# Performance work log

Hardware: AMD Instinct MI355X
Metric: run time of the kernel (lower is better)

## Reference

```python
import jax, jax.numpy as jnp
import numpy as np

PREV_SIZE = 1024
SIZE = 4096
BATCH = 8192


def setup_inputs() -> dict:
    key = jax.random.key(0)
    k1, k2, k3, k4 = jax.random.split(key, 4)
    return {
        "prev_layer_output": jax.random.normal(k1, (PREV_SIZE, BATCH), dtype=jnp.float32),
        "input_A_weights": jax.random.normal(k2, (SIZE, PREV_SIZE), dtype=jnp.float32),
        "input_B_weights": jax.random.normal(k3, (SIZE, PREV_SIZE), dtype=jnp.float32),
        "table_weights": jax.random.normal(k4, (16, SIZE), dtype=jnp.float32),
    }


def reference(prev_layer_output, input_A_weights, input_B_weights, table_weights):
    # Soft input selection via row-softmax over previous neurons.
    pa = jax.nn.softmax(input_A_weights, axis=1)   # (size, prev_size)
    pb = jax.nn.softmax(input_B_weights, axis=1)   # (size, prev_size)
    pt = jax.nn.softmax(table_weights, axis=0)     # (16, size) softmax over gates

    A = pa @ prev_layer_output                     # (size, batch)
    B = pb @ prev_layer_output                     # (size, batch)
    AB = A * B

    p = pt[:, :, None]                             # (16, size, 1) broadcast over batch
    # Fused weighted sum over the 16 soft logic gates (no (16,size,batch) buffer).
    out = (
        p[1] * AB
        + p[2] * (A - AB)
        + p[3] * A
        + p[4] * (B - AB)
        + p[5] * B
        + p[6] * (A + B - 2.0 * AB)
        + p[7] * (A + B - AB)
        + p[8] * (1.0 - (A + B - AB))
        + p[9] * (1.0 - (A + B - 2.0 * AB))
        + p[10] * (1.0 - B)
        + p[11] * (1.0 - B + AB)
        + p[12] * (1.0 - A)
        + p[13] * (1.0 - A + AB)
        + p[14] * (1.0 - AB)
        + p[15]
    )
    return out
```

## Files before the change

kernel.cpp:

```cpp
#include <hip/hip_runtime.h>
#include <hip/hip_bf16.h>

#define K_DIM 1024
#define M_DIM 4096
#define N_DIM 8192
#define BK 64
#define BM 128
#define BN 256
#define NT 16

#define OFF_A 0
#define OFF_B (BM * BK)
#define OFF_P (2 * BM * BK)
#define BUF_ELEMS (2 * BM * BK + BN * BK)

typedef __attribute__((ext_vector_type(8))) __bf16 bf16x8_t;
typedef __attribute__((ext_vector_type(4))) float f32x4;

#define SBAR do { __builtin_amdgcn_sched_barrier(0); \
                  __builtin_amdgcn_s_barrier(); \
                  __builtin_amdgcn_sched_barrier(0); } while (0)
#define LGKM0 do { asm volatile("s_waitcnt lgkmcnt(0)" ::: "memory"); \
                   __builtin_amdgcn_sched_barrier(0); } while (0)
#define VMCNT(n) do { asm volatile("s_waitcnt vmcnt(" #n ")" ::: "memory"); \
                      __builtin_amdgcn_sched_barrier(0); } while (0)

__device__ inline unsigned short f2bf(float f) {
    unsigned u = __float_as_uint(f);
    u += 0x7FFF + ((u >> 16) & 1);
    return (unsigned short)(u >> 16);
}

__device__ __forceinline__ void gload_lds16(const void* g, void* l) {
    __builtin_amdgcn_global_load_lds(
        (const __attribute__((address_space(1))) unsigned int*)g,
        (__attribute__((address_space(3))) unsigned int*)l, 16, 0, 0);
}

__global__ void dual_softmax_kernel(const float* __restrict__ wa,
                                    const float* __restrict__ wb,
                                    unsigned short* __restrict__ pa,
                                    unsigned short* __restrict__ pb) {
    const int idx = blockIdx.x;
    const float* w = (idx < M_DIM) ? wa : wb;
    unsigned short* o = (idx < M_DIM) ? pa : pb;
    const int row = idx & (M_DIM - 1);
    const int tid = threadIdx.x;
    const float4 v = reinterpret_cast<const float4*>(w + (size_t)row * K_DIM)[tid];
    float m = fmaxf(fmaxf(v.x, v.y), fmaxf(v.z, v.w));
    #pragma unroll
    for (int off = 32; off >= 1; off >>= 1) m = fmaxf(m, __shfl_xor(m, off));
    __shared__ float redm[4];
    __shared__ float reds[4];
    if ((tid & 63) == 0) redm[tid >> 6] = m;
    __syncthreads();
    m = fmaxf(fmaxf(redm[0], redm[1]), fmaxf(redm[2], redm[3]));
    const float e0 = __expf(v.x - m), e1 = __expf(v.y - m);
    const float e2 = __expf(v.z - m), e3 = __expf(v.w - m);
    float s = e0 + e1 + e2 + e3;
    #pragma unroll
    for (int off = 32; off >= 1; off >>= 1) s += __shfl_xor(s, off);
    if ((tid & 63) == 0) reds[tid >> 6] = s;
    __syncthreads();
    s = reds[0] + reds[1] + reds[2] + reds[3];
    const float inv = 1.0f / s;
    ushort4 r;
    r.x = f2bf(e0 * inv); r.y = f2bf(e1 * inv);
    r.z = f2bf(e2 * inv); r.w = f2bf(e3 * inv);
    reinterpret_cast<ushort4*>(o + (size_t)row * K_DIM)[tid] = r;
}

__global__ void transpose_conv_kernel(const float* __restrict__ src,
                                      unsigned short* __restrict__ dst) {
    __shared__ float t[32][33];
    const int n0 = blockIdx.x * 32;
    const int k0 = blockIdx.y * 32;
    const int tx = threadIdx.x, ty = threadIdx.y;
    #pragma unroll
    for (int i = ty; i < 32; i += 8)
        t[i][tx] = src[(size_t)(k0 + i) * N_DIM + n0 + tx];
    __syncthreads();
    #pragma unroll
    for (int i = ty; i < 32; i += 8)
        dst[(size_t)(n0 + i) * K_DIM + k0 + tx] = f2bf(t[tx][i]);
}

__global__ void coef_kernel(const float* __restrict__ tw,
                            float4* __restrict__ coef) {
    const int r = blockIdx.x * 256 + threadIdx.x;
    float p[16];
    float m = -1e30f;
    #pragma unroll
    for (int k = 0; k < 16; ++k) { p[k] = tw[k * M_DIM + r]; m = fmaxf(m, p[k]); }
    float s = 0.f;
    #pragma unroll
    for (int k = 0; k < 16; ++k) { p[k] = __expf(p[k] - m); s += p[k]; }
    const float inv = 1.f / s;
    #pragma unroll
    for (int k = 0; k < 16; ++k) p[k] *= inv;
    const float cA  = p[2]+p[3]+p[6]+p[7]-p[8]-p[9]-p[12]-p[13];
    const float cB  = p[4]+p[5]+p[6]+p[7]-p[8]-p[9]-p[10]-p[11];
    const float cAB = p[1]-p[2]-p[4]-2.f*p[6]-p[7]+p[8]+2.f*p[9]+p[11]+p[13]-p[14];
    const float c0  = p[8]+p[9]+p[10]+p[11]+p[12]+p[13]+p[14]+p[15];
    coef[r] = make_float4(cA, cB, cAB, c0);
}

__device__ __forceinline__ void load_frags4(const unsigned short* lbase, int row0,
                                            int fk16, bf16x8_t (&f)[4]) {
    #pragma unroll
    for (int i = 0; i < 4; ++i) {
        const int row = row0 + i * 16;
        f[i] = *reinterpret_cast<const bf16x8_t*>(
            (const char*)lbase + row * 128 + ((fk16 ^ (row & 7)) * 16));
    }
}

__device__ __forceinline__ void mfma_block(const bf16x8_t (&a)[4], const bf16x8_t (&p)[4],
                                           f32x4 (&acc)[4][4]) {
    #pragma unroll
    for (int mi = 0; mi < 4; ++mi)
        #pragma unroll
        for (int ni = 0; ni < 4; ++ni)
            acc[mi][ni] = __builtin_amdgcn_mfma_f32_16x16x32_bf16(
                a[mi], p[ni], acc[mi][ni], 0, 0, 0);
}

__global__ __launch_bounds__(512, 2)
void dual_gemm_kernel(const unsigned short* __restrict__ pa,
                      const unsigned short* __restrict__ pb,
                      const unsigned short* __restrict__ pv,
                      const float4* __restrict__ coef,
                      float* __restrict__ out) {
    __shared__ unsigned short lds[2 * BUF_ELEMS];

    const int tid = threadIdx.x;
    const int lane = tid & 63;
    const int w = tid >> 6;
    const int wm = w >> 2, wn = w & 3;

    const int bm = blockIdx.y;
    const int bn = blockIdx.x;

    const int sub_row = lane >> 3;
    const int scol16  = (lane & 7) ^ sub_row;

    const unsigned short* gA = pa + (size_t)(bm * BM) * K_DIM;
    const unsigned short* gB = pb + (size_t)(bm * BM) * K_DIM;
    const unsigned short* gP = pv + (size_t)(bn * BN) * K_DIM;

    const int fr  = lane & 15;
    const int fkb = lane >> 4;
    const int arow0 = wm * 64 + fr;
    const int prow0 = wn * 64 + fr;

    f32x4 accA[4][4], accB[4][4];
    const f32x4 z = {0.f, 0.f, 0.f, 0.f};
    #pragma unroll
    for (int i = 0; i < 4; ++i)
        #pragma unroll
        for (int j = 0; j < 4; ++j) { accA[i][j] = z; accB[i][j] = z; }

    auto stage = [&](const unsigned short* gbase, int lds_elem_off, int chunk, int k) {
        const int r = chunk * 8 + sub_row;
        const char* src = (const char*)(gbase + (size_t)r * K_DIM + k) + scol16 * 16;
        char* dst = (char*)&lds[lds_elem_off] + chunk * 1024;
        gload_lds16(src, dst);
    };

    stage(gA, OFF_A, 2 * w, 0);     stage(gA, OFF_A, 2 * w + 1, 0);
    stage(gP, OFF_P, 4 * w, 0);     stage(gP, OFF_P, 4 * w + 1, 0);
    stage(gP, OFF_P, 4 * w + 2, 0); stage(gP, OFF_P, 4 * w + 3, 0);
    stage(gB, OFF_B, 2 * w, 0);     stage(gB, OFF_B, 2 * w + 1, 0);
    VMCNT(2);
    SBAR;

    for (int t = 0; t < NT - 1; ++t) {
        const int kn = (t + 1) * BK;
        const int co = (t & 1) * BUF_ELEMS;
        const int no = co ^ BUF_ELEMS;
        bf16x8_t af[4], pf[4], bfv[4];

        load_frags4(&lds[co + OFF_A], arow0, fkb, af);
        load_frags4(&lds[co + OFF_P], prow0, fkb, pf);
        stage(gA, no + OFF_A, 2 * w, kn); stage(gA, no + OFF_A, 2 * w + 1, kn);
        stage(gP, no + OFF_P, 4 * w, kn); stage(gP, no + OFF_P, 4 * w + 1, kn);
        stage(gP, no + OFF_P, 4 * w + 2, kn); stage(gP, no + OFF_P, 4 * w + 3, kn);
        VMCNT(6);
        SBAR;
        LGKM0;
        __builtin_amdgcn_s_setprio(1);
        mfma_block(af, pf, accA);
        __builtin_amdgcn_s_setprio(0);
        SBAR;

        load_frags4(&lds[co + OFF_B], arow0, fkb, bfv);
        stage(gB, no + OFF_B, 2 * w, kn); stage(gB, no + OFF_B, 2 * w + 1, kn);
        SBAR;
        LGKM0;
        __builtin_amdgcn_s_setprio(1);
        mfma_block(bfv, pf, accB);
        __builtin_amdgcn_s_setprio(0);
        SBAR;

        load_frags4(&lds[co + OFF_A], arow0, fkb + 4, af);
        load_frags4(&lds[co + OFF_P], prow0, fkb + 4, pf);
        SBAR;
        LGKM0;
        __builtin_amdgcn_s_setprio(1);
        mfma_block(af, pf, accA);
        __builtin_amdgcn_s_setprio(0);
        SBAR;

        load_frags4(&lds[co + OFF_B], arow0, fkb + 4, bfv);
        VMCNT(2);
        SBAR;
        LGKM0;
        __builtin_amdgcn_s_setprio(1);
        mfma_block(bfv, pf, accB);
        __builtin_amdgcn_s_setprio(0);
        SBAR;
    }

    {
        const int co = ((NT - 1) & 1) * BUF_ELEMS;
        bf16x8_t af[4], pf[4], bfv[4];
        load_frags4(&lds[co + OFF_A], arow0, fkb, af);
        load_frags4(&lds[co + OFF_P], prow0, fkb, pf);
        VMCNT(0);
        SBAR;
        LGKM0;
        __builtin_amdgcn_s_setprio(1);
        mfma_block(af, pf, accA);
        __builtin_amdgcn_s_setprio(0);
        load_frags4(&lds[co + OFF_B], arow0, fkb, bfv);
        mfma_block(bfv, pf, accB);
        load_frags4(&lds[co + OFF_A], arow0, fkb + 4, af);
        load_frags4(&lds[co + OFF_P], prow0, fkb + 4, pf);
        mfma_block(af, pf, accA);
        load_frags4(&lds[co + OFF_B], arow0, fkb + 4, bfv);
        mfma_block(bfv, pf, accB);
    }

    const int row_grp = lane >> 4;
    #pragma unroll
    for (int mi = 0; mi < 4; ++mi) {
        #pragma unroll
        for (int ni = 0; ni < 4; ++ni) {
            const int gr0 = bm * BM + wm * 64 + mi * 16 + row_grp * 4;
            const int gc  = bn * BN + wn * 64 + ni * 16 + (lane & 15);
            #pragma unroll
            for (int i = 0; i < 4; ++i) {
                const int r = gr0 + i;
                const float4 cf = coef[r];
                const float av = accA[mi][ni][i];
                const float bv = accB[mi][ni][i];
                out[(size_t)r * N_DIM + gc] =
                    fmaf(cf.z, av * bv, fmaf(cf.x, av, fmaf(cf.y, bv, cf.w)));
            }
        }
    }
}

extern "C" void kernel_launch(void* const* d_in, const int* in_sizes, int n_in,
                              void* d_out, int out_size, void* d_ws, size_t ws_size,
                              hipStream_t stream) {
    const float* prev = (const float*)d_in[0];
    const float* wa   = (const float*)d_in[1];
    const float* wb   = (const float*)d_in[2];
    const float* tw   = (const float*)d_in[3];
    float* out = (float*)d_out;

    char* ws = (char*)d_ws;
    unsigned short* pa = (unsigned short*)ws;
    unsigned short* pb = (unsigned short*)(ws + 8388608);
    unsigned short* pv = (unsigned short*)(ws + 16777216);
    float4* coef       = (float4*)(ws + 33554432);

    dual_softmax_kernel<<<2 * M_DIM, 256, 0, stream>>>(wa, wb, pa, pb);
    transpose_conv_kernel<<<dim3(N_DIM / 32, K_DIM / 32), dim3(32, 8), 0, stream>>>(prev, pv);
    coef_kernel<<<M_DIM / 256, 256, 0, stream>>>(tw, coef);
    dual_gemm_kernel<<<dim3(N_DIM / BN, M_DIM / BM), 512, 0, stream>>>(pa, pb, pv, coef, out);
}
```

Measured before the change: 155.0 us.

## Double-buffer register fragments to overlap LDS reads with MFMA blocks

Restructures the main K loop so that LDS fragment loads for the next MFMA block are issued before the current MFMA block runs. Two sets of register fragments are used, and the next tile's first A/P fragments are prefetched at the end of each iteration. This is meant to hide LDS read latency behind matrix math and to remove some barriers. In exchange it raises register pressure, which may cut occupancy, and it adds a full VMCNT(0) wait each iteration.

```diff
diff --git a/kernel.cpp b/kernel.cpp
--- a/kernel.cpp
+++ b/kernel.cpp
@@ -24,6 +24,7 @@
                    __builtin_amdgcn_sched_barrier(0); } while (0)
 #define VMCNT(n) do { asm volatile("s_waitcnt vmcnt(" #n ")" ::: "memory"); \
                       __builtin_amdgcn_sched_barrier(0); } while (0)
+#define SCHED_FENCE __builtin_amdgcn_sched_barrier(0)
 
 __device__ inline unsigned short f2bf(float f) {
     unsigned u = __float_as_uint(f);
@@ -167,78 +168,81 @@
         gload_lds16(src, dst);
     };
 
+    bf16x8_t af0[4], pf0[4], bf0[4], af1[4], pf1[4], bf1[4];
+
     stage(gA, OFF_A, 2 * w, 0);     stage(gA, OFF_A, 2 * w + 1, 0);
     stage(gP, OFF_P, 4 * w, 0);     stage(gP, OFF_P, 4 * w + 1, 0);
     stage(gP, OFF_P, 4 * w + 2, 0); stage(gP, OFF_P, 4 * w + 3, 0);
     stage(gB, OFF_B, 2 * w, 0);     stage(gB, OFF_B, 2 * w + 1, 0);
-    VMCNT(2);
+    VMCNT(0);
     SBAR;
+    load_frags4(&lds[OFF_A], arow0, fkb, af0);
+    load_frags4(&lds[OFF_P], prow0, fkb, pf0);
+    SCHED_FENCE;
 
     for (int t = 0; t < NT - 1; ++t) {
         const int kn = (t + 1) * BK;
         const int co = (t & 1) * BUF_ELEMS;
         const int no = co ^ BUF_ELEMS;
-        bf16x8_t af[4], pf[4], bfv[4];
-
-        load_frags4(&lds[co + OFF_A], arow0, fkb, af);
-        load_frags4(&lds[co + OFF_P], prow0, fkb, pf);
+
         stage(gA, no + OFF_A, 2 * w, kn); stage(gA, no + OFF_A, 2 * w + 1, kn);
         stage(gP, no + OFF_P, 4 * w, kn); stage(gP, no + OFF_P, 4 * w + 1, kn);
         stage(gP, no + OFF_P, 4 * w + 2, kn); stage(gP, no + OFF_P, 4 * w + 3, kn);
-        VMCNT(6);
-        SBAR;
-        LGKM0;
-        __builtin_amdgcn_s_setprio(1);
-        mfma_block(af, pf, accA);
-        __builtin_amdgcn_s_setprio(0);
-        SBAR;
-
-        load_frags4(&lds[co + OFF_B], arow0, fkb, bfv);
+        LGKM0;
+        load_frags4(&lds[co + OFF_B], arow0, fkb, bf0);
+        SCHED_FENCE;
+        __builtin_amdgcn_s_setprio(1);
+        mfma_block(af0, pf0, accA);
+        __builtin_amdgcn_s_setprio(0);
+        SBAR;
+
         stage(gB, no + OFF_B, 2 * w, kn); stage(gB, no + OFF_B, 2 * w + 1, kn);
-        SBAR;
-        LGKM0;
-        __builtin_amdgcn_s_setprio(1);
-        mfma_block(bfv, pf, accB);
-        __builtin_amdgcn_s_setprio(0);
-        SBAR;
-
-        load_frags4(&lds[co + OFF_A], arow0, fkb + 4, af);
-        load_frags4(&lds[co + OFF_P], prow0, fkb + 4, pf);
-        SBAR;
-        LGKM0;
-        __builtin_amdgcn_s_setprio(1);
-        mfma_block(af, pf, accA);
-        __builtin_amdgcn_s_setprio(0);
-        SBAR;
-
-        load_frags4(&lds[co + OFF_B], arow0, fkb + 4, bfv);
+        LGKM0;
+        load_frags4(&lds[co + OFF_A], arow0, fkb + 4, af1);
+        load_frags4(&lds[co + OFF_P], prow0, fkb + 4, pf1);
+        SCHED_FENCE;
+        __builtin_amdgcn_s_setprio(1);
+        mfma_block(bf0, pf0, accB);
+        __builtin_amdgcn_s_setprio(0);
+        SBAR;
+
         VMCNT(2);
-        SBAR;
-        LGKM0;
-        __builtin_amdgcn_s_setprio(1);
-        mfma_block(bfv, pf, accB);
+        LGKM0;
+        load_frags4(&lds[co + OFF_B], arow0, fkb + 4, bf1);
+        SCHED_FENCE;
+        __builtin_amdgcn_s_setprio(1);
+        mfma_block(af1, pf1, accA);
+        __builtin_amdgcn_s_setprio(0);
+        SBAR;
+
+        VMCNT(0);
+        LGKM0;
+        load_frags4(&lds[no + OFF_A], arow0, fkb, af0);
+        load_frags4(&lds[no + OFF_P], prow0, fkb, pf0);
+        SCHED_FENCE;
+        __builtin_amdgcn_s_setprio(1);
+        mfma_block(bf1, pf1, accB);
         __builtin_amdgcn_s_setprio(0);
         SBAR;
     }
 
     {
         const int co = ((NT - 1) & 1) * BUF_ELEMS;
-        bf16x8_t af[4], pf[4], bfv[4];
-        load_frags4(&lds[co + OFF_A], arow0, fkb, af);
-        load_frags4(&lds[co + OFF_P], prow0, fkb, pf);
-        VMCNT(0);
-        SBAR;
-        LGKM0;
-        __builtin_amdgcn_s_setprio(1);
-        mfma_block(af, pf, accA);
-        __builtin_amdgcn_s_setprio(0);
-        load_frags4(&lds[co + OFF_B], arow0, fkb, bfv);
-        mfma_block(bfv, pf, accB);
-        load_frags4(&lds[co + OFF_A], arow0, fkb + 4, af);
-        load_frags4(&lds[co + OFF_P], prow0, fkb + 4, pf);
-        mfma_block(af, pf, accA);
-        load_frags4(&lds[co + OFF_B], arow0, fkb + 4, bfv);
-        mfma_block(bfv, pf, accB);
+        LGKM0;
+        load_frags4(&lds[co + OFF_B], arow0, fkb, bf0);
+        SCHED_FENCE;
+        mfma_block(af0, pf0, accA);
+        LGKM0;
+        load_frags4(&lds[co + OFF_A], arow0, fkb + 4, af1);
+        load_frags4(&lds[co + OFF_P], prow0, fkb + 4, pf1);
+        SCHED_FENCE;
+        mfma_block(bf0, pf0, accB);
+        LGKM0;
+        load_frags4(&lds[co + OFF_B], arow0, fkb + 4, bf1);
+        SCHED_FENCE;
+        mfma_block(af1, pf1, accA);
+        LGKM0;
+        mfma_block(bf1, pf1, accB);
     }
 
     const int row_grp = lane >> 4;
```

New measurement: 155.1 us. No clear change (+0.0%).
